# Performance work log

Measured on AMD Instinct MI355X. Metric: run time of the kernel, lower is better.

## Reference

```python
import jax, jax.numpy as jnp
import numpy as np

N_NODES = 140000   # 14 frames * 10000 nodes/frame
N_EDGES = 2240000  # avg degree 16
NFEAT = 128
NHID = 128
N_FRAMES = 14


def setup_inputs() -> dict:
    key = jax.random.key(0)
    k1, k2, k3, k4, k5 = jax.random.split(key, 5)
    x = jax.random.normal(k1, (N_NODES, NFEAT), dtype=jnp.float32)
    # gc1 parameters (only layer actually used in forward)
    W = jax.random.normal(k2, (NFEAT, NHID), dtype=jnp.float32) * 0.05
    b = jnp.zeros((NHID,), dtype=jnp.float32)
    # sparse normalized adjacency as COO edge list (row sorted for fast segment_sum)
    edge_row = jnp.sort(jax.random.randint(k3, (N_EDGES,), 0, N_NODES, dtype=jnp.int32))
    edge_col = jax.random.randint(k4, (N_EDGES,), 0, N_NODES, dtype=jnp.int32)
    edge_val = jax.random.uniform(k5, (N_EDGES,), dtype=jnp.float32)
    return {"x": x, "W": W, "b": b, "edge_val": edge_val,
            "edge_row": edge_row, "edge_col": edge_col}


def reference(x, W, b, edge_val, edge_row, edge_col):
    # GraphConvolution: adj @ (x @ W) + b  (adj sparse, COO)
    support = x @ W                                   # [N, NHID]
    msgs = edge_val[:, None] * support[edge_col]      # [E, NHID] gather
    agg = jax.ops.segment_sum(msgs, edge_row, num_segments=N_NODES,
                              indices_are_sorted=True)  # [N, NHID] scatter-add
    h = jax.nn.relu(agg + b)
    # view(14, -1, c) then max over frame axis
    h = h.reshape(N_FRAMES, -1, NHID)                 # [14, N/14, NHID]
    h = jnp.max(h, axis=0)                            # [N/14, NHID]
    return jax.nn.log_softmax(h, axis=1)
```

## Files before the change

kernel.cpp:

```cpp
#include <hip/hip_runtime.h>
#include <hip/hip_bf16.h>

#define N_NODES 140000
#define N_EDGES 2240000
#define NFEAT 128
#define NHID 128
#define N_FRAMES 14
#define NODES_PER_FRAME 10000
#define CAP 352

typedef __attribute__((ext_vector_type(8))) short frag_b16;
typedef __attribute__((ext_vector_type(4))) int frag_i4;
typedef __attribute__((ext_vector_type(4))) float f32x4;

__device__ __forceinline__ unsigned short f2bf(float f) {
    union { float f; unsigned int u; } v; v.f = f;
    unsigned int r = v.u + 0x7fffu + ((v.u >> 16) & 1u);
    return (unsigned short)(r >> 16);
}
__device__ __forceinline__ int pk_bf16(float a, float b) {
    union { __hip_bfloat162 h; int i; } u;
    u.h = __float22bfloat162_rn(make_float2(a, b));
    return u.i;
}

__global__ void prep_kernel(const float* __restrict__ W, unsigned short* __restrict__ WT,
                            const int* __restrict__ edge_row, int* __restrict__ row_ptr) {
    int e = blockIdx.x * blockDim.x + threadIdx.x;
    if (e < NFEAT * NHID) {
        int k = e >> 7, n = e & 127;
        WT[n * 128 + k] = f2bf(W[e]);
    }
    if (e < N_EDGES) {
        int r = edge_row[e];
        int prev = (e == 0) ? -1 : edge_row[e - 1];
        for (int q = prev + 1; q <= r; ++q) row_ptr[q] = e;
        if (e == N_EDGES - 1) {
            for (int q = r + 1; q <= N_NODES; ++q) row_ptr[q] = N_EDGES;
        }
    }
}

#define WT_STRIDE 136

__global__ __launch_bounds__(256) void gemm_kernel(
        const float* __restrict__ x, const unsigned short* __restrict__ WT,
        unsigned char* __restrict__ supQ, float* __restrict__ scales) {
    __shared__ unsigned short wt_lds[128 * WT_STRIDE];

    const uint4* WTv = (const uint4*)WT;
    for (int idx = threadIdx.x; idx < 2048; idx += 256) {
        uint4 d = WTv[idx];
        int elem = idx << 3;
        int n = elem >> 7, k = elem & 127;
        *(uint4*)&wt_lds[n * WT_STRIDE + k] = d;
    }

    int wave = threadIdx.x >> 6;
    int lane = threadIdx.x & 63;
    int m = lane & 15;
    int q = lane >> 4;

    long row0 = (long)blockIdx.x * 64 + wave * 16;

    int arow = (int)row0 + m;
    if (arow >= N_NODES) arow = N_NODES - 1;
    const float* xrow = x + (long)arow * 128 + q * 8;
    frag_b16 xa[4];
#pragma unroll
    for (int ks = 0; ks < 4; ++ks) {
        float4 lo = *(const float4*)(xrow + ks * 32);
        float4 hi = *(const float4*)(xrow + ks * 32 + 4);
        union { frag_b16 f; frag_i4 i; } u;
        u.i[0] = pk_bf16(lo.x, lo.y);
        u.i[1] = pk_bf16(lo.z, lo.w);
        u.i[2] = pk_bf16(hi.x, hi.y);
        u.i[3] = pk_bf16(hi.z, hi.w);
        xa[ks] = u.f;
    }

    __syncthreads();

    if (row0 < N_NODES) {
        f32x4 acc[8];
#pragma unroll
        for (int t = 0; t < 8; ++t) acc[t] = (f32x4){0.f, 0.f, 0.f, 0.f};

#pragma unroll
        for (int t = 0; t < 8; ++t) {
            const unsigned short* bp = &wt_lds[(t * 16 + m) * WT_STRIDE + q * 8];
#pragma unroll
            for (int ks = 0; ks < 4; ++ks) {
                frag_b16 wfrag = *(const frag_b16*)(bp + ks * 32);
                acc[t] = __builtin_amdgcn_mfma_f32_16x16x32_bf16(wfrag, xa[ks], acc[t], 0, 0, 0);
            }
        }

        float amax = 0.f;
#pragma unroll
        for (int t = 0; t < 8; ++t)
#pragma unroll
            for (int r = 0; r < 4; ++r) amax = fmaxf(amax, fabsf(acc[t][r]));
        amax = fmaxf(amax, __shfl_xor(amax, 16));
        amax = fmaxf(amax, __shfl_xor(amax, 32));
        float rinv = amax > 0.f ? 127.f / amax : 0.f;

        long node = row0 + m;
        if (node < N_NODES) {
            if (q == 0) scales[node] = amax * (1.f / 127.f);
            unsigned char* srow = supQ + node * 128;
#pragma unroll
            for (int t = 0; t < 8; ++t) {
                unsigned u0 = (unsigned)(rintf(acc[t][0] * rinv) + 128.f);
                unsigned u1 = (unsigned)(rintf(acc[t][1] * rinv) + 128.f);
                unsigned u2 = (unsigned)(rintf(acc[t][2] * rinv) + 128.f);
                unsigned u3 = (unsigned)(rintf(acc[t][3] * rinv) + 128.f);
                *(unsigned*)(srow + t * 16 + q * 4) = u0 | (u1 << 8) | (u2 << 16) | (u3 << 24);
            }
        }
    }
}

__global__ __launch_bounds__(128) void agg_kernel(
        const unsigned char* __restrict__ supQ, const float* __restrict__ scales,
        const float* __restrict__ b,
        const float* __restrict__ edge_val, const int* __restrict__ edge_col,
        const int* __restrict__ row_ptr, float* __restrict__ out) {
    __shared__ int    segStart[2][8];
    __shared__ int    segLen[2][8];
    __shared__ int    segOff[2][8];
    __shared__ int2   eBuf[2][CAP];
    __shared__ float4 xch[2][32];

    const int i = blockIdx.x;
    const int lane = threadIdx.x & 63;
    const int w = threadIdx.x >> 6;
    const int eh = lane >> 5;
    const int f4 = lane & 31;
    const unsigned f4x4 = (unsigned)f4 * 4u;

    int a = 0, len = 0;
    if (lane < 7) {
        int n = (w * 7 + lane) * NODES_PER_FRAME + i;
        a = row_ptr[n];
        len = row_ptr[n + 1] - a;
    }
    int len8 = (len + 7) & ~7;
    int off = 0;
#pragma unroll
    for (int f2 = 0; f2 < 7; ++f2) {
        int L2 = __shfl(len8, f2);
        if (f2 < lane) off += L2;
    }
    if (lane < 7) { segStart[w][lane] = a; segLen[w][lane] = len; segOff[w][lane] = off; }
    if (lane == 6) segOff[w][7] = off + len8;
    __syncthreads();

    const bool fit = segOff[w][7] <= CAP;

    if (fit) {
#pragma unroll 1
        for (int f = 0; f < 7; ++f) {
            int g = segStart[w][f], s = segOff[w][f], L = segLen[w][f];
            int L8 = (L + 7) & ~7;
            for (int j = lane; j < L8; j += 64) {
                int2 v = make_int2(0, 0);
                if (j < L) {
                    int c = edge_col[g + j];
                    v.x = c;
                    v.y = __float_as_int(edge_val[g + j] * scales[c]);
                }
                eBuf[w][s + j] = v;
            }
        }
    }
    __syncthreads();

    const float4 bb = *(const float4*)&b[f4 * 4];
    float4 mx = make_float4(0.f, 0.f, 0.f, 0.f);

    if (fit) {
#pragma unroll 1
        for (int f = 0; f < 7; ++f) {
            int s = segOff[w][f];
            int e8 = s + ((segLen[w][f] + 7) & ~7);
            float a0 = 0.f, a1 = 0.f, a2 = 0.f, a3 = 0.f, svf = 0.f;
            for (int j = s; j < e8; j += 8) {
                int2 ed[4];
#pragma unroll
                for (int p = 0; p < 4; ++p) ed[p] = eBuf[w][j + 2 * p + eh];
                unsigned q4[4];
#pragma unroll
                for (int p = 0; p < 4; ++p)
                    q4[p] = *(const unsigned*)(supQ + (((unsigned)ed[p].x) << 7) + f4x4);
#pragma unroll
                for (int p = 0; p < 4; ++p) {
                    float vp = __int_as_float(ed[p].y);
                    a0 = fmaf(vp, (float)( q4[p]        & 0xffu), a0);
                    a1 = fmaf(vp, (float)((q4[p] >> 8)  & 0xffu), a1);
                    a2 = fmaf(vp, (float)((q4[p] >> 16) & 0xffu), a2);
                    a3 = fmaf(vp, (float)( q4[p] >> 24        ), a3);
                    svf += vp;
                }
            }
            a0 += __shfl_xor(a0, 32); a1 += __shfl_xor(a1, 32);
            a2 += __shfl_xor(a2, 32); a3 += __shfl_xor(a3, 32);
            svf += __shfl_xor(svf, 32);
            float h0 = fmaf(-128.f, svf, a0) + bb.x;
            float h1 = fmaf(-128.f, svf, a1) + bb.y;
            float h2 = fmaf(-128.f, svf, a2) + bb.z;
            float h3 = fmaf(-128.f, svf, a3) + bb.w;
            mx.x = fmaxf(mx.x, fmaxf(h0, 0.f));
            mx.y = fmaxf(mx.y, fmaxf(h1, 0.f));
            mx.z = fmaxf(mx.z, fmaxf(h2, 0.f));
            mx.w = fmaxf(mx.w, fmaxf(h3, 0.f));
        }
    } else {
#pragma unroll 1
        for (int f = 0; f < 7; ++f) {
            int g = segStart[w][f], L = segLen[w][f];
            float a0 = 0.f, a1 = 0.f, a2 = 0.f, a3 = 0.f, svf = 0.f;
            for (int j = eh; j < L; j += 2) {
                int c = edge_col[g + j];
                float vp = edge_val[g + j] * scales[c];
                unsigned qv = *(const unsigned*)(supQ + (((unsigned)c) << 7) + f4x4);
                a0 = fmaf(vp, (float)( qv        & 0xffu), a0);
                a1 = fmaf(vp, (float)((qv >> 8)  & 0xffu), a1);
                a2 = fmaf(vp, (float)((qv >> 16) & 0xffu), a2);
                a3 = fmaf(vp, (float)( qv >> 24        ), a3);
                svf += vp;
            }
            a0 += __shfl_xor(a0, 32); a1 += __shfl_xor(a1, 32);
            a2 += __shfl_xor(a2, 32); a3 += __shfl_xor(a3, 32);
            svf += __shfl_xor(svf, 32);
            float h0 = fmaf(-128.f, svf, a0) + bb.x;
            float h1 = fmaf(-128.f, svf, a1) + bb.y;
            float h2 = fmaf(-128.f, svf, a2) + bb.z;
            float h3 = fmaf(-128.f, svf, a3) + bb.w;
            mx.x = fmaxf(mx.x, fmaxf(h0, 0.f));
            mx.y = fmaxf(mx.y, fmaxf(h1, 0.f));
            mx.z = fmaxf(mx.z, fmaxf(h2, 0.f));
            mx.w = fmaxf(mx.w, fmaxf(h3, 0.f));
        }
    }

    if (eh == 0) xch[w][f4] = mx;
    __syncthreads();
    float4 m0 = xch[0][f4], m1 = xch[1][f4];
    float o0 = fmaxf(m0.x, m1.x);
    float o1 = fmaxf(m0.y, m1.y);
    float o2 = fmaxf(m0.z, m1.z);
    float o3 = fmaxf(m0.w, m1.w);

    float M = fmaxf(fmaxf(o0, o1), fmaxf(o2, o3));
#pragma unroll
    for (int o = 16; o >= 1; o >>= 1) M = fmaxf(M, __shfl_xor(M, o));
    float S = __expf(o0 - M) + __expf(o1 - M) + __expf(o2 - M) + __expf(o3 - M);
#pragma unroll
    for (int o = 16; o >= 1; o >>= 1) S += __shfl_xor(S, o);

    if (w == 0 && eh == 0) {
        float ls = __logf(S);
        *(float4*)&out[i * 128 + f4 * 4] =
            make_float4(o0 - M - ls, o1 - M - ls, o2 - M - ls, o3 - M - ls);
    }
}

extern "C" void kernel_launch(void* const* d_in, const int* in_sizes, int n_in,
                              void* d_out, int out_size, void* d_ws, size_t ws_size,
                              hipStream_t stream) {
    const float* x        = (const float*)d_in[0];
    const float* W        = (const float*)d_in[1];
    const float* b        = (const float*)d_in[2];
    const float* edge_val = (const float*)d_in[3];
    const int*   edge_row = (const int*)d_in[4];
    const int*   edge_col = (const int*)d_in[5];
    float* out = (float*)d_out;

    char* ws = (char*)d_ws;
    unsigned char*  supQ    = (unsigned char*)ws;
    float*          scales  = (float*)(ws + 17920000);
    unsigned short* WT      = (unsigned short*)(ws + 18480000);
    int*            row_ptr = (int*)(ws + 18512768);

    prep_kernel<<<(N_EDGES + 255) / 256, 256, 0, stream>>>(W, WT, edge_row, row_ptr);
    gemm_kernel<<<(N_NODES + 63) / 64, 256, 0, stream>>>(x, WT, supQ, scales);
    agg_kernel<<<NODES_PER_FRAME, 128, 0, stream>>>(supQ, scales, b, edge_val, edge_col, row_ptr, out);
}
```

Measured before the change: 198.7 us.

## Precompute scaled edge values and widen aggregation gathers to 8 bytes

Splits the weight conversion into its own kernel and moves CSR construction after the GEMM, so the prep kernel can also precompute edge_val*scales[col] into a per-edge array. The aggregation kernel then reads the precomputed values instead of gathering scales. Each lane now covers 8 features with a uint2 gather, so four edges are processed in parallel per wave instead of two. This halves the number of gather instructions per edge row but adds an extra 9 MB write/read pass, an extra kernel launch, and an extra shuffle stage in the reduction.

```diff
diff --git a/kernel.cpp b/kernel.cpp
--- a/kernel.cpp
+++ b/kernel.cpp
@@ -24,21 +24,11 @@
     return u.i;
 }
 
-__global__ void prep_kernel(const float* __restrict__ W, unsigned short* __restrict__ WT,
-                            const int* __restrict__ edge_row, int* __restrict__ row_ptr) {
-    int e = blockIdx.x * blockDim.x + threadIdx.x;
-    if (e < NFEAT * NHID) {
-        int k = e >> 7, n = e & 127;
-        WT[n * 128 + k] = f2bf(W[e]);
-    }
-    if (e < N_EDGES) {
-        int r = edge_row[e];
-        int prev = (e == 0) ? -1 : edge_row[e - 1];
-        for (int q = prev + 1; q <= r; ++q) row_ptr[q] = e;
-        if (e == N_EDGES - 1) {
-            for (int q = r + 1; q <= N_NODES; ++q) row_ptr[q] = N_EDGES;
-        }
-    }
+__global__ void convert_wt(const float* __restrict__ W, unsigned short* __restrict__ WT) {
+    int idx = blockIdx.x * blockDim.x + threadIdx.x;
+    if (idx >= NFEAT * NHID) return;
+    int k = idx >> 7, n = idx & 127;
+    WT[n * 128 + k] = f2bf(W[idx]);
 }
 
 #define WT_STRIDE 136
@@ -121,23 +111,36 @@
     }
 }
 
+__global__ void prep_kernel(const int* __restrict__ edge_row, const int* __restrict__ edge_col,
+                            const float* __restrict__ edge_val, const float* __restrict__ scales,
+                            int* __restrict__ row_ptr, float* __restrict__ valp) {
+    int e = blockIdx.x * blockDim.x + threadIdx.x;
+    if (e >= N_EDGES) return;
+    int r = edge_row[e];
+    int prev = (e == 0) ? -1 : edge_row[e - 1];
+    for (int q = prev + 1; q <= r; ++q) row_ptr[q] = e;
+    if (e == N_EDGES - 1) {
+        for (int q = r + 1; q <= N_NODES; ++q) row_ptr[q] = N_EDGES;
+    }
+    valp[e] = edge_val[e] * scales[edge_col[e]];
+}
+
 __global__ __launch_bounds__(128) void agg_kernel(
-        const unsigned char* __restrict__ supQ, const float* __restrict__ scales,
-        const float* __restrict__ b,
-        const float* __restrict__ edge_val, const int* __restrict__ edge_col,
+        const unsigned char* __restrict__ supQ, const float* __restrict__ b,
+        const float* __restrict__ valp, const int* __restrict__ edge_col,
         const int* __restrict__ row_ptr, float* __restrict__ out) {
     __shared__ int    segStart[2][8];
     __shared__ int    segLen[2][8];
     __shared__ int    segOff[2][8];
     __shared__ int2   eBuf[2][CAP];
-    __shared__ float4 xch[2][32];
+    __shared__ float4 xch[2][16][2];
 
     const int i = blockIdx.x;
     const int lane = threadIdx.x & 63;
     const int w = threadIdx.x >> 6;
-    const int eh = lane >> 5;
-    const int f4 = lane & 31;
-    const unsigned f4x4 = (unsigned)f4 * 4u;
+    const int eh = lane >> 4;
+    const int f8 = lane & 15;
+    const unsigned f8x8 = (unsigned)f8 * 8u;
 
     int a = 0, len = 0;
     if (lane < 7) {
@@ -166,9 +169,8 @@
             for (int j = lane; j < L8; j += 64) {
                 int2 v = make_int2(0, 0);
                 if (j < L) {
-                    int c = edge_col[g + j];
-                    v.x = c;
-                    v.y = __float_as_int(edge_val[g + j] * scales[c]);
+                    v.x = edge_col[g + j];
+                    v.y = __float_as_int(valp[g + j]);
                 }
                 eBuf[w][s + j] = v;
             }
@@ -176,93 +178,138 @@
     }
     __syncthreads();
 
-    const float4 bb = *(const float4*)&b[f4 * 4];
-    float4 mx = make_float4(0.f, 0.f, 0.f, 0.f);
+    const float4 blo = *(const float4*)&b[f8 * 8];
+    const float4 bhi = *(const float4*)&b[f8 * 8 + 4];
+    float m0 = 0.f, m1 = 0.f, m2 = 0.f, m3 = 0.f;
+    float m4 = 0.f, m5 = 0.f, m6 = 0.f, m7 = 0.f;
 
     if (fit) {
 #pragma unroll 1
         for (int f = 0; f < 7; ++f) {
             int s = segOff[w][f];
             int e8 = s + ((segLen[w][f] + 7) & ~7);
-            float a0 = 0.f, a1 = 0.f, a2 = 0.f, a3 = 0.f, svf = 0.f;
+            float a0 = 0.f, a1 = 0.f, a2 = 0.f, a3 = 0.f;
+            float a4 = 0.f, a5 = 0.f, a6 = 0.f, a7 = 0.f, svf = 0.f;
             for (int j = s; j < e8; j += 8) {
-                int2 ed[4];
-#pragma unroll
-                for (int p = 0; p < 4; ++p) ed[p] = eBuf[w][j + 2 * p + eh];
-                unsigned q4[4];
-#pragma unroll
-                for (int p = 0; p < 4; ++p)
-                    q4[p] = *(const unsigned*)(supQ + (((unsigned)ed[p].x) << 7) + f4x4);
-#pragma unroll
-                for (int p = 0; p < 4; ++p) {
-                    float vp = __int_as_float(ed[p].y);
-                    a0 = fmaf(vp, (float)( q4[p]        & 0xffu), a0);
-                    a1 = fmaf(vp, (float)((q4[p] >> 8)  & 0xffu), a1);
-                    a2 = fmaf(vp, (float)((q4[p] >> 16) & 0xffu), a2);
-                    a3 = fmaf(vp, (float)( q4[p] >> 24        ), a3);
-                    svf += vp;
-                }
-            }
+                int2 e0 = eBuf[w][j + eh];
+                int2 e1 = eBuf[w][j + 4 + eh];
+                uint2 q0 = *(const uint2*)(supQ + (((unsigned)e0.x) << 7) + f8x8);
+                uint2 q1 = *(const uint2*)(supQ + (((unsigned)e1.x) << 7) + f8x8);
+                float v0 = __int_as_float(e0.y);
+                float v1 = __int_as_float(e1.y);
+                a0 = fmaf(v0, (float)( q0.x        & 0xffu), a0);
+                a1 = fmaf(v0, (float)((q0.x >> 8)  & 0xffu), a1);
+                a2 = fmaf(v0, (float)((q0.x >> 16) & 0xffu), a2);
+                a3 = fmaf(v0, (float)( q0.x >> 24        ), a3);
+                a4 = fmaf(v0, (float)( q0.y        & 0xffu), a4);
+                a5 = fmaf(v0, (float)((q0.y >> 8)  & 0xffu), a5);
+                a6 = fmaf(v0, (float)((q0.y >> 16) & 0xffu), a6);
+                a7 = fmaf(v0, (float)( q0.y >> 24        ), a7);
+                svf += v0;
+                a0 = fmaf(v1, (float)( q1.x        & 0xffu), a0);
+                a1 = fmaf(v1, (float)((q1.x >> 8)  & 0xffu), a1);
+                a2 = fmaf(v1, (float)((q1.x >> 16) & 0xffu), a2);
+                a3 = fmaf(v1, (float)( q1.x >> 24        ), a3);
+                a4 = fmaf(v1, (float)( q1.y        & 0xffu), a4);
+                a5 = fmaf(v1, (float)((q1.y >> 8)  & 0xffu), a5);
+                a6 = fmaf(v1, (float)((q1.y >> 16) & 0xffu), a6);
+                a7 = fmaf(v1, (float)( q1.y >> 24        ), a7);
+                svf += v1;
+            }
+            a0 += __shfl_xor(a0, 16); a1 += __shfl_xor(a1, 16);
+            a2 += __shfl_xor(a2, 16); a3 += __shfl_xor(a3, 16);
+            a4 += __shfl_xor(a4, 16); a5 += __shfl_xor(a5, 16);
+            a6 += __shfl_xor(a6, 16); a7 += __shfl_xor(a7, 16);
+            svf += __shfl_xor(svf, 16);
             a0 += __shfl_xor(a0, 32); a1 += __shfl_xor(a1, 32);
             a2 += __shfl_xor(a2, 32); a3 += __shfl_xor(a3, 32);
+            a4 += __shfl_xor(a4, 32); a5 += __shfl_xor(a5, 32);
+            a6 += __shfl_xor(a6, 32); a7 += __shfl_xor(a7, 32);
             svf += __shfl_xor(svf, 32);
-            float h0 = fmaf(-128.f, svf, a0) + bb.x;
-            float h1 = fmaf(-128.f, svf, a1) + bb.y;
-            float h2 = fmaf(-128.f, svf, a2) + bb.z;
-            float h3 = fmaf(-128.f, svf, a3) + bb.w;
-            mx.x = fmaxf(mx.x, fmaxf(h0, 0.f));
-            mx.y = fmaxf(mx.y, fmaxf(h1, 0.f));
-            mx.z = fmaxf(mx.z, fmaxf(h2, 0.f));
-            mx.w = fmaxf(mx.w, fmaxf(h3, 0.f));
+            float h0 = fmaf(-128.f, svf, a0) + blo.x;
+            float h1 = fmaf(-128.f, svf, a1) + blo.y;
+            float h2 = fmaf(-128.f, svf, a2) + blo.z;
+            float h3 = fmaf(-128.f, svf, a3) + blo.w;
+            float h4 = fmaf(-128.f, svf, a4) + bhi.x;
+            float h5 = fmaf(-128.f, svf, a5) + bhi.y;
+            float h6 = fmaf(-128.f, svf, a6) + bhi.z;
+            float h7 = fmaf(-128.f, svf, a7) + bhi.w;
+            m0 = fmaxf(m0, fmaxf(h0, 0.f)); m1 = fmaxf(m1, fmaxf(h1, 0.f));
+            m2 = fmaxf(m2, fmaxf(h2, 0.f)); m3 = fmaxf(m3, fmaxf(h3, 0.f));
+            m4 = fmaxf(m4, fmaxf(h4, 0.f)); m5 = fmaxf(m5, fmaxf(h5, 0.f));
+            m6 = fmaxf(m6, fmaxf(h6, 0.f)); m7 = fmaxf(m7, fmaxf(h7, 0.f));
         }
     } else {
 #pragma unroll 1
         for (int f = 0; f < 7; ++f) {
             int g = segStart[w][f], L = segLen[w][f];
-            float a0 = 0.f, a1 = 0.f, a2 = 0.f, a3 = 0.f, svf = 0.f;
-            for (int j = eh; j < L; j += 2) {
+            float a0 = 0.f, a1 = 0.f, a2 = 0.f, a3 = 0.f;
+            float a4 = 0.f, a5 = 0.f, a6 = 0.f, a7 = 0.f, svf = 0.f;
+            for (int j = eh; j < L; j += 4) {
                 int c = edge_col[g + j];
-                float vp = edge_val[g + j] * scales[c];
-                unsigned qv = *(const unsigned*)(supQ + (((unsigned)c) << 7) + f4x4);
-                a0 = fmaf(vp, (float)( qv        & 0xffu), a0);
-                a1 = fmaf(vp, (float)((qv >> 8)  & 0xffu), a1);
-                a2 = fmaf(vp, (float)((qv >> 16) & 0xffu), a2);
-                a3 = fmaf(vp, (float)( qv >> 24        ), a3);
-                svf += vp;
-            }
+                float v = valp[g + j];
+                uint2 qv = *(const uint2*)(supQ + (((unsigned)c) << 7) + f8x8);
+                a0 = fmaf(v, (float)( qv.x        & 0xffu), a0);
+                a1 = fmaf(v, (float)((qv.x >> 8)  & 0xffu), a1);
+                a2 = fmaf(v, (float)((qv.x >> 16) & 0xffu), a2);
+                a3 = fmaf(v, (float)( qv.x >> 24        ), a3);
+                a4 = fmaf(v, (float)( qv.y        & 0xffu), a4);
+                a5 = fmaf(v, (float)((qv.y >> 8)  & 0xffu), a5);
+                a6 = fmaf(v, (float)((qv.y >> 16) & 0xffu), a6);
+                a7 = fmaf(v, (float)( qv.y >> 24        ), a7);
+                svf += v;
+            }
+            a0 += __shfl_xor(a0, 16); a1 += __shfl_xor(a1, 16);
+            a2 += __shfl_xor(a2, 16); a3 += __shfl_xor(a3, 16);
+            a4 += __shfl_xor(a4, 16); a5 += __shfl_xor(a5, 16);
+            a6 += __shfl_xor(a6, 16); a7 += __shfl_xor(a7, 16);
+            svf += __shfl_xor(svf, 16);
             a0 += __shfl_xor(a0, 32); a1 += __shfl_xor(a1, 32);
             a2 += __shfl_xor(a2, 32); a3 += __shfl_xor(a3, 32);
+            a4 += __shfl_xor(a4, 32); a5 += __shfl_xor(a5, 32);
+            a6 += __shfl_xor(a6, 32); a7 += __shfl_xor(a7, 32);
             svf += __shfl_xor(svf, 32);
-            float h0 = fmaf(-128.f, svf, a0) + bb.x;
-            float h1 = fmaf(-128.f, svf, a1) + bb.y;
-            float h2 = fmaf(-128.f, svf, a2) + bb.z;
-            float h3 = fmaf(-128.f, svf, a3) + bb.w;
-            mx.x = fmaxf(mx.x, fmaxf(h0, 0.f));
-            mx.y = fmaxf(mx.y, fmaxf(h1, 0.f));
-            mx.z = fmaxf(mx.z, fmaxf(h2, 0.f));
-            mx.w = fmaxf(mx.w, fmaxf(h3, 0.f));
-        }
-    }
-
-    if (eh == 0) xch[w][f4] = mx;
+            float h0 = fmaf(-128.f, svf, a0) + blo.x;
+            float h1 = fmaf(-128.f, svf, a1) + blo.y;
+            float h2 = fmaf(-128.f, svf, a2) + blo.z;
+            float h3 = fmaf(-128.f, svf, a3) + blo.w;
+            float h4 = fmaf(-128.f, svf, a4) + bhi.x;
+            float h5 = fmaf(-128.f, svf, a5) + bhi.y;
+            float h6 = fmaf(-128.f, svf, a6) + bhi.z;
+            float h7 = fmaf(-128.f, svf, a7) + bhi.w;
+            m0 = fmaxf(m0, fmaxf(h0, 0.f)); m1 = fmaxf(m1, fmaxf(h1, 0.f));
+            m2 = fmaxf(m2, fmaxf(h2, 0.f)); m3 = fmaxf(m3, fmaxf(h3, 0.f));
+            m4 = fmaxf(m4, fmaxf(h4, 0.f)); m5 = fmaxf(m5, fmaxf(h5, 0.f));
+            m6 = fmaxf(m6, fmaxf(h6, 0.f)); m7 = fmaxf(m7, fmaxf(h7, 0.f));
+        }
+    }
+
+    if (eh == 0) {
+        xch[w][f8][0] = make_float4(m0, m1, m2, m3);
+        xch[w][f8][1] = make_float4(m4, m5, m6, m7);
+    }
     __syncthreads();
-    float4 m0 = xch[0][f4], m1 = xch[1][f4];
-    float o0 = fmaxf(m0.x, m1.x);
-    float o1 = fmaxf(m0.y, m1.y);
-    float o2 = fmaxf(m0.z, m1.z);
-    float o3 = fmaxf(m0.w, m1.w);
-
-    float M = fmaxf(fmaxf(o0, o1), fmaxf(o2, o3));
-#pragma unroll
-    for (int o = 16; o >= 1; o >>= 1) M = fmaxf(M, __shfl_xor(M, o));
-    float S = __expf(o0 - M) + __expf(o1 - M) + __expf(o2 - M) + __expf(o3 - M);
-#pragma unroll
-    for (int o = 16; o >= 1; o >>= 1) S += __shfl_xor(S, o);
+    float4 p0 = xch[0][f8][0], p1 = xch[0][f8][1];
+    float4 q0 = xch[1][f8][0], q1 = xch[1][f8][1];
+    float o0 = fmaxf(p0.x, q0.x), o1 = fmaxf(p0.y, q0.y);
+    float o2 = fmaxf(p0.z, q0.z), o3 = fmaxf(p0.w, q0.w);
+    float o4 = fmaxf(p1.x, q1.x), o5 = fmaxf(p1.y, q1.y);
+    float o6 = fmaxf(p1.z, q1.z), o7 = fmaxf(p1.w, q1.w);
+
+    float M = fmaxf(fmaxf(fmaxf(o0, o1), fmaxf(o2, o3)),
+                    fmaxf(fmaxf(o4, o5), fmaxf(o6, o7)));
+#pragma unroll
+    for (int o = 8; o >= 1; o >>= 1) M = fmaxf(M, __shfl_xor(M, o));
+    float S = __expf(o0 - M) + __expf(o1 - M) + __expf(o2 - M) + __expf(o3 - M)
+            + __expf(o4 - M) + __expf(o5 - M) + __expf(o6 - M) + __expf(o7 - M);
+#pragma unroll
+    for (int o = 8; o >= 1; o >>= 1) S += __shfl_xor(S, o);
 
     if (w == 0 && eh == 0) {
         float ls = __logf(S);
-        *(float4*)&out[i * 128 + f4 * 4] =
-            make_float4(o0 - M - ls, o1 - M - ls, o2 - M - ls, o3 - M - ls);
+        float* orow = out + i * 128 + f8 * 8;
+        *(float4*)orow       = make_float4(o0 - M - ls, o1 - M - ls, o2 - M - ls, o3 - M - ls);
+        *(float4*)(orow + 4) = make_float4(o4 - M - ls, o5 - M - ls, o6 - M - ls, o7 - M - ls);
     }
 }
 
@@ -282,8 +329,11 @@
     float*          scales  = (float*)(ws + 17920000);
     unsigned short* WT      = (unsigned short*)(ws + 18480000);
     int*            row_ptr = (int*)(ws + 18512768);
-
-    prep_kernel<<<(N_EDGES + 255) / 256, 256, 0, stream>>>(W, WT, edge_row, row_ptr);
+    float*          valp    = (float*)(ws + 19072772);
+
+    convert_wt<<<64, 256, 0, stream>>>(W, WT);
     gemm_kernel<<<(N_NODES + 63) / 64, 256, 0, stream>>>(x, WT, supQ, scales);
-    agg_kernel<<<NODES_PER_FRAME, 128, 0, stream>>>(supQ, scales, b, edge_val, edge_col, row_ptr, out);
-}
+    prep_kernel<<<(N_EDGES + 255) / 256, 256, 0, stream>>>(edge_row, edge_col, edge_val,
+                                                           scales, row_ptr, valp);
+    agg_kernel<<<NODES_PER_FRAME, 128, 0, stream>>>(supQ, b, valp, edge_col, row_ptr, out);
+}
```

After: 213.0 us. 1.07x slower.
